# Kernel optimization log

Measured on AMD Instinct MI355X. Metric: run time of the kernel, lower is better.

The kernel has to match this reference:

```python
import jax, jax.numpy as jnp
import numpy as np

L, H, D, FF = 12, 12, 768, 3072          # ViT-B/16
PS, GRID = 16, 14
NP = GRID * GRID                          # 196 patches
NT = NP + 1                               # 197 tokens (cls + patches)
B = 64
NC = 100                                  # classes
POS_G = (0, 1)
POS_E = (2, 3, 4)
LEN_G, LEN_E = 5, 20
GL, EL = len(POS_G), len(POS_E)
E_POOL = 10                               # task_num


def _ln(x, g, b, eps=1e-6):
    m = x.mean(-1, keepdims=True)
    v = ((x - m) ** 2).mean(-1, keepdims=True)
    return (x - m) * jax.lax.rsqrt(v + eps) * g + b


def _mlp(x, w1, b1, w2, b2):
    return jax.nn.gelu(x @ w1.T + b1, approximate=False) @ w2.T + b2


def _attn(q, k, v):
    # q: [B,Nq,C], k/v: [B,Nk,C] (Nk may include prefix prompt tokens)
    Bq, Nq, C = q.shape
    hd = C // H
    q = q.reshape(Bq, Nq, H, hd).transpose(0, 2, 1, 3)
    k = k.reshape(Bq, -1, H, hd).transpose(0, 2, 1, 3)
    v = v.reshape(Bq, -1, H, hd).transpose(0, 2, 1, 3)
    a = jax.nn.softmax(jnp.einsum('bhqd,bhkd->bhqk', q, k) * (hd ** -0.5), axis=-1)
    o = jnp.einsum('bhqk,bhkd->bhqd', a, v)
    return o.transpose(0, 2, 1, 3).reshape(Bq, Nq, C)


def setup_inputs() -> dict:
    key = jax.random.key(0)
    ks = iter(jax.random.split(key, 24))
    s = 0.02
    return {
        'inputs':    jax.random.normal(next(ks), (B, 3, 224, 224), jnp.float32),
        'patch_w':   jax.random.normal(next(ks), (D, 3, PS, PS), jnp.float32) * s,
        'patch_b':   jnp.zeros((D,), jnp.float32),
        'cls_token': jax.random.normal(next(ks), (1, 1, D), jnp.float32) * s,
        'pos_embed': jax.random.normal(next(ks), (1, NT, D), jnp.float32) * s,
        'ln1_g':  jnp.ones((L, D), jnp.float32),
        'ln1_b':  jnp.zeros((L, D), jnp.float32),
        'qkv_w':  jax.random.normal(next(ks), (L, 3 * D, D), jnp.float32) * s,
        'qkv_b':  jnp.zeros((L, 3 * D), jnp.float32),
        'proj_w': jax.random.normal(next(ks), (L, D, D), jnp.float32) * s,
        'proj_b': jnp.zeros((L, D), jnp.float32),
        'ln2_g':  jnp.ones((L, D), jnp.float32),
        'ln2_b':  jnp.zeros((L, D), jnp.float32),
        'fc1_w':  jax.random.normal(next(ks), (L, FF, D), jnp.float32) * s,
        'fc1_b':  jnp.zeros((L, FF), jnp.float32),
        'fc2_w':  jax.random.normal(next(ks), (L, D, FF), jnp.float32) * s,
        'fc2_b':  jnp.zeros((L, D), jnp.float32),
        'norm_g': jnp.ones((D,), jnp.float32),
        'norm_b': jnp.zeros((D,), jnp.float32),
        'head_w': jax.random.normal(next(ks), (NC, D), jnp.float32) * s,
        'head_b': jnp.zeros((NC,), jnp.float32),
        'g_prompt': jax.random.normal(next(ks), (1, 2 * GL * LEN_G, D), jnp.float32) * s,
        'e_key':    jax.random.normal(next(ks), (E_POOL, D), jnp.float32),
        'e_prompt': jax.random.normal(next(ks), (E_POOL, 2 * EL * LEN_E, D), jnp.float32) * s,
    }


def _forward(inputs, patch_w, patch_b, cls_token, pos_embed, ln1_g, ln1_b,
             qkv_w, qkv_b, proj_w, proj_b, ln2_g, ln2_b, fc1_w, fc1_b,
             fc2_w, fc2_b, norm_g, norm_b, head_w, head_b,
             g_prompt, e_key, e_prompt):
    Bn = inputs.shape[0]
    # --- patch embed (conv k16 s16 == unfold + linear); under torch.no_grad ---
    x = inputs.reshape(Bn, 3, GRID, PS, GRID, PS).transpose(0, 2, 4, 1, 3, 5)
    x = x.reshape(Bn, NP, 3 * PS * PS) @ patch_w.reshape(D, -1).T + patch_b
    tok = jnp.concatenate([jnp.broadcast_to(cls_token, (Bn, 1, D)), x], axis=1)
    tok = jax.lax.stop_gradient(tok)  # token_appended computed in no_grad block
    # --- frozen query pass through plain ViT blocks ---
    q = tok + pos_embed
    for i in range(L):
        xn = _ln(q, ln1_g[i], ln1_b[i])
        qq, kk, vv = jnp.split(xn @ qkv_w[i].T + qkv_b[i], 3, axis=-1)
        q = q + _attn(qq, kk, vv) @ proj_w[i].T + proj_b[i]
        q = q + _mlp(_ln(q, ln2_g[i], ln2_b[i]), fc1_w[i], fc1_b[i], fc2_w[i], fc2_b[i])
    query = jax.lax.stop_gradient(_ln(q, norm_g, norm_b)[:, 0])  # [B, D]
    # --- prompt selection (eval path: cosine-sim top-1 from e-pool) ---
    qn = query / jnp.linalg.norm(query, axis=-1, keepdims=True)
    kn = e_key / jnp.linalg.norm(e_key, axis=-1, keepdims=True)
    idx = jnp.argmax(qn @ kn.T, axis=-1)                       # [B]
    cls_pe = pos_embed[0, 0]                                   # [D]
    g_p = jnp.broadcast_to(g_prompt[0].reshape(1, 2 * GL, LEN_G, D),
                           (Bn, 2 * GL, LEN_G, D)) + cls_pe
    e_p = e_prompt[idx].reshape(Bn, 2 * EL, LEN_E, D) + cls_pe
    # --- prefix-tuning pass: prompts concatenated to K/V only ---
    x = tok + pos_embed
    for n in range(L):
        xn = _ln(x, ln1_g[n], ln1_b[n])
        ks_, vs_ = [xn], [xn]
        if n in POS_G:
            j = POS_G.index(n)
            ks_.append(g_p[:, 2 * j]); vs_.append(g_p[:, 2 * j + 1])
        if n in POS_E:
            j = POS_E.index(n)
            ks_.append(e_p[:, 2 * j]); vs_.append(e_p[:, 2 * j + 1])
        xk = jnp.concatenate(ks_, axis=1) if len(ks_) > 1 else xn
        xv = jnp.concatenate(vs_, axis=1) if len(vs_) > 1 else xn
        qh = xn @ qkv_w[n][:D].T + qkv_b[n][:D]
        kh = xk @ qkv_w[n][D:2 * D].T + qkv_b[n][D:2 * D]
        vh = xv @ qkv_w[n][2 * D:].T + qkv_b[n][2 * D:]
        x = x + _attn(qh, kh, vh) @ proj_w[n].T + proj_b[n]
        x = x + _mlp(_ln(x, ln2_g[n], ln2_b[n]), fc1_w[n], fc1_b[n], fc2_w[n], fc2_b[n])
    x = _ln(x, norm_g, norm_b)
    return x[:, 0] @ head_w.T + head_b  # [B, NC]


def reference(inputs, patch_w, patch_b, cls_token, pos_embed, ln1_g, ln1_b,
              qkv_w, qkv_b, proj_w, proj_b, ln2_g, ln2_b, fc1_w, fc1_b,
              fc2_w, fc2_b, norm_g, norm_b, head_w, head_b,
              g_prompt, e_key, e_prompt):
    return _forward(inputs, patch_w, patch_b, cls_token, pos_embed, ln1_g, ln1_b,
                    qkv_w, qkv_b, proj_w, proj_b, ln2_g, ln2_b, fc1_w, fc1_b,
                    fc2_w, fc2_b, norm_g, norm_b, head_w, head_b,
                    g_prompt, e_key, e_prompt)
```

## Files before the change

kernel.cpp:

```cpp
#include <hip/hip_runtime.h>

typedef unsigned short ushort_t;
typedef __attribute__((ext_vector_type(8))) __bf16 bf16x8;
typedef __attribute__((ext_vector_type(4))) float f32x4;
typedef __attribute__((ext_vector_type(4))) unsigned int u32x4;
typedef __attribute__((ext_vector_type(4))) unsigned short u16x4;
typedef __attribute__((ext_vector_type(4))) float fl4;

#define AS1(p) ((const __attribute__((address_space(1))) void*)(p))
#define AS3(p) ((__attribute__((address_space(3))) void*)(p))

__device__ __forceinline__ ushort_t f2bf(float f) {
    unsigned u = __float_as_uint(f);
    u += 0x7FFFu + ((u >> 16) & 1u);
    return (ushort_t)(u >> 16);
}

__device__ __forceinline__ bf16x8 ld_bf8(const ushort_t* p) {
    return __builtin_bit_cast(bf16x8, *(const u32x4*)p);
}

__device__ __forceinline__ float gelu_f(float x) {
    float z = 1.5957691216057308f * (x + 0.044715f * x * x * x);
    float e = __expf(z);
    return x * e / (e + 1.f);
}

__global__ void cvt_kernel(const float* __restrict__ in, ushort_t* __restrict__ out, int n4)
{
    int i = blockIdx.x * 256 + threadIdx.x;
    if (i >= n4) return;
    fl4 f = ((const fl4*)in)[i];
    u16x4 h;
    h.x = f2bf(f.x); h.y = f2bf(f.y); h.z = f2bf(f.z); h.w = f2bf(f.w);
    ((u16x4*)out)[i] = h;
}

template<int OBF, int ADD, int GELU>
__global__ __launch_bounds__(256)
void gemm_kernel(const ushort_t* __restrict__ A, const ushort_t* __restrict__ W,
                 const float* __restrict__ bias, void* __restrict__ Cv,
                 int M, int N, int K, int ntiles)
{
    __shared__ ushort_t As[128 * 32];
    __shared__ ushort_t Ws[128 * 32];
    const int tid  = threadIdx.x;
    const int lane = tid & 63, wv = tid >> 6;
    const int quad = lane >> 4, l16 = lane & 15;

    const int mtiles = gridDim.x / ntiles;
    const int GM = 8;
    int gsz = GM * ntiles;
    int grp = blockIdx.x / gsz;
    int fm  = grp * GM;
    int gm  = min(GM, mtiles - fm);
    int ing = blockIdx.x - grp * gsz;
    const int m0 = (fm + ing % gm) * 128;
    const int n0 = (ing / gm) * 128;

    const int wm = (wv >> 1) * 64, wn = (wv & 1) * 64;

    f32x4 acc[4][4];
#pragma unroll
    for (int j = 0; j < 4; ++j)
#pragma unroll
        for (int i = 0; i < 4; ++i) acc[j][i] = (f32x4){0.f, 0.f, 0.f, 0.f};

    const int lr = lane >> 2, lc = (lane & 3) * 8;
    const ushort_t* gA0 = A + (size_t)(m0 + wv * 16 + lr) * K + lc;
    const ushort_t* gA1 = gA0 + (size_t)64 * K;
    const ushort_t* gW0 = W + (size_t)(n0 + wv * 16 + lr) * K + lc;
    const ushort_t* gW1 = gW0 + (size_t)64 * K;
    ushort_t* lA0 = As + wv * 512;
    ushort_t* lA1 = As + (wv + 4) * 512;
    ushort_t* lW0 = Ws + wv * 512;
    ushort_t* lW1 = Ws + (wv + 4) * 512;

    for (int kt = 0; kt < K; kt += 32) {
        __builtin_amdgcn_global_load_lds(AS1(gA0 + kt), AS3(lA0), 16, 0, 0);
        __builtin_amdgcn_global_load_lds(AS1(gA1 + kt), AS3(lA1), 16, 0, 0);
        __builtin_amdgcn_global_load_lds(AS1(gW0 + kt), AS3(lW0), 16, 0, 0);
        __builtin_amdgcn_global_load_lds(AS1(gW1 + kt), AS3(lW1), 16, 0, 0);
        __syncthreads();
        bf16x8 af[4], bfr[4];
#pragma unroll
        for (int i = 0; i < 4; ++i) af[i]  = ld_bf8(As + (wm + i * 16 + l16) * 32 + quad * 8);
#pragma unroll
        for (int j = 0; j < 4; ++j) bfr[j] = ld_bf8(Ws + (wn + j * 16 + l16) * 32 + quad * 8);
#pragma unroll
        for (int j = 0; j < 4; ++j)
#pragma unroll
            for (int i = 0; i < 4; ++i)
                acc[j][i] = __builtin_amdgcn_mfma_f32_16x16x32_bf16(bfr[j], af[i], acc[j][i], 0, 0, 0);
        __syncthreads();
    }

    float* Cf = (float*)Cv;
    ushort_t* Ch = (ushort_t*)Cv;
    fl4 bv[4];
#pragma unroll
    for (int j = 0; j < 4; ++j) bv[j] = *(const fl4*)(bias + n0 + wn + j * 16 + quad * 4);

#pragma unroll
    for (int i = 0; i < 4; ++i) {
        int m = m0 + wm + i * 16 + l16;
        if (m >= M) continue;
        size_t rowoff = (size_t)m * N;
#pragma unroll
        for (int j = 0; j < 4; ++j) {
            int nb = n0 + wn + j * 16 + quad * 4;
            float vals[4];
#pragma unroll
            for (int r = 0; r < 4; ++r) {
                float v = acc[j][i][r] + bv[j][r];
                if (GELU) v = gelu_f(v);
                vals[r] = v;
            }
            if (OBF) {
                u16x4 h;
                h.x = f2bf(vals[0]); h.y = f2bf(vals[1]);
                h.z = f2bf(vals[2]); h.w = f2bf(vals[3]);
                *(u16x4*)(Ch + rowoff + nb) = h;
            } else {
                fl4 o = {vals[0], vals[1], vals[2], vals[3]};
                if (ADD) {
                    fl4 c = *(const fl4*)(Cf + rowoff + nb);
                    o.x += c.x; o.y += c.y; o.z += c.z; o.w += c.w;
                }
                *(fl4*)(Cf + rowoff + nb) = o;
            }
        }
    }
}

__global__ __launch_bounds__(256)
void attn_kernel(const ushort_t* __restrict__ qkv, const ushort_t* __restrict__ pk,
                 const ushort_t* __restrict__ pv, int plen, int pbs,
                 ushort_t* __restrict__ out)
{
    __shared__ ushort_t KV[224 * 72];
    __shared__ ushort_t Ps[64 * 232];
    const int tid  = threadIdx.x;
    const int lane = tid & 63, wv = tid >> 6;
    const int quad = lane >> 4, l16 = lane & 15;
    const int b = blockIdx.x / 12, h = blockIdx.x % 12;
    const int q0 = blockIdx.y * 64;
    const int Nk = 197 + plen;

    for (int i = tid; i < 224 * 8; i += 256) {
        int tok = i >> 3, c = (i & 7) * 8;
        u32x4 v = (u32x4){0, 0, 0, 0};
        if (tok < 197)
            v = *(const u32x4*)(qkv + (size_t)(b * 197 + tok) * 2304 + 768 + h * 64 + c);
        else if (tok < Nk)
            v = *(const u32x4*)(pk + (size_t)(b * pbs + (tok - 197)) * 768 + h * 64 + c);
        *(u32x4*)(KV + tok * 72 + c) = v;
    }
    __syncthreads();

    bf16x8 qf0 = __builtin_bit_cast(bf16x8, (u32x4){0, 0, 0, 0});
    bf16x8 qf1 = qf0;
    int qrow = q0 + wv * 16 + l16;
    if (qrow < 197) {
        const ushort_t* qp = qkv + (size_t)(b * 197 + qrow) * 2304 + h * 64 + quad * 8;
        qf0 = ld_bf8(qp);
        qf1 = ld_bf8(qp + 32);
    }

    f32x4 sarr[14];
#pragma unroll
    for (int t = 0; t < 14; ++t) {
        f32x4 s = (f32x4){0.f, 0.f, 0.f, 0.f};
        bf16x8 k0 = ld_bf8(KV + (t * 16 + l16) * 72 + quad * 8);
        bf16x8 k1 = ld_bf8(KV + (t * 16 + l16) * 72 + 32 + quad * 8);
        s = __builtin_amdgcn_mfma_f32_16x16x32_bf16(qf0, k0, s, 0, 0, 0);
        s = __builtin_amdgcn_mfma_f32_16x16x32_bf16(qf1, k1, s, 0, 0, 0);
        if (t * 16 + l16 >= Nk) s = (f32x4){-1e30f, -1e30f, -1e30f, -1e30f};
        sarr[t] = s;
    }

    float mx[4] = {-1e30f, -1e30f, -1e30f, -1e30f};
#pragma unroll
    for (int t = 0; t < 14; ++t)
#pragma unroll
        for (int r = 0; r < 4; ++r) mx[r] = fmaxf(mx[r], sarr[t][r]);
#pragma unroll
    for (int off = 8; off >= 1; off >>= 1)
#pragma unroll
        for (int r = 0; r < 4; ++r) mx[r] = fmaxf(mx[r], __shfl_xor(mx[r], off));

    float sm[4] = {0.f, 0.f, 0.f, 0.f};
#pragma unroll
    for (int t = 0; t < 14; ++t)
#pragma unroll
        for (int r = 0; r < 4; ++r) {
            float p = __expf((sarr[t][r] - mx[r]) * 0.125f);
            sm[r] += p;
            Ps[(wv * 16 + quad * 4 + r) * 232 + t * 16 + l16] = f2bf(p);
        }
#pragma unroll
    for (int off = 8; off >= 1; off >>= 1)
#pragma unroll
        for (int r = 0; r < 4; ++r) sm[r] += __shfl_xor(sm[r], off);
    float rs[4];
#pragma unroll
    for (int r = 0; r < 4; ++r) rs[r] = 1.f / sm[r];
    __syncthreads();

    for (int i = tid; i < 224 * 8; i += 256) {
        int tok = i >> 3, c = (i & 7) * 8;
        u32x4 v = (u32x4){0, 0, 0, 0};
        if (tok < 197)
            v = *(const u32x4*)(qkv + (size_t)(b * 197 + tok) * 2304 + 1536 + h * 64 + c);
        else if (tok < Nk)
            v = *(const u32x4*)(pv + (size_t)(b * pbs + (tok - 197)) * 768 + h * 64 + c);
        ushort_t tmp[8];
        *(u32x4*)tmp = v;
#pragma unroll
        for (int jj = 0; jj < 8; ++jj) KV[(c + jj) * 232 + tok] = tmp[jj];
    }
    __syncthreads();

    f32x4 oc[4];
#pragma unroll
    for (int j = 0; j < 4; ++j) oc[j] = (f32x4){0.f, 0.f, 0.f, 0.f};
#pragma unroll
    for (int ks = 0; ks < 7; ++ks) {
        bf16x8 pf = ld_bf8(Ps + (wv * 16 + l16) * 232 + ks * 32 + quad * 8);
#pragma unroll
        for (int j = 0; j < 4; ++j) {
            bf16x8 vf = ld_bf8(KV + (j * 16 + l16) * 232 + ks * 32 + quad * 8);
            oc[j] = __builtin_amdgcn_mfma_f32_16x16x32_bf16(pf, vf, oc[j], 0, 0, 0);
        }
    }
#pragma unroll
    for (int j = 0; j < 4; ++j) {
        int hd = h * 64 + j * 16 + l16;
#pragma unroll
        for (int r = 0; r < 4; ++r) {
            int qr = q0 + wv * 16 + quad * 4 + r;
            if (qr < 197) out[(size_t)(b * 197 + qr) * 768 + hd] = f2bf(oc[j][r] * rs[r]);
        }
    }
}

__global__ __launch_bounds__(256)
void ln_kernel(const float* __restrict__ x, const float* __restrict__ g,
               const float* __restrict__ bt, ushort_t* __restrict__ out)
{
    const int row = blockIdx.x, tid = threadIdx.x;
    const float* xr = x + (size_t)row * 768;
    float v0 = xr[tid], v1 = xr[tid + 256], v2 = xr[tid + 512];
    float s = v0 + v1 + v2;
    float s2 = v0 * v0 + v1 * v1 + v2 * v2;
#pragma unroll
    for (int off = 32; off >= 1; off >>= 1) {
        s  += __shfl_xor(s, off);
        s2 += __shfl_xor(s2, off);
    }
    __shared__ float red[8];
    if ((tid & 63) == 0) { red[tid >> 6] = s; red[(tid >> 6) + 4] = s2; }
    __syncthreads();
    float S  = red[0] + red[1] + red[2] + red[3];
    float S2 = red[4] + red[5] + red[6] + red[7];
    float mean = S * (1.f / 768.f);
    float var  = fmaxf(S2 * (1.f / 768.f) - mean * mean, 0.f);
    float rstd = rsqrtf(var + 1e-6f);
    size_t o = (size_t)row * 768;
    out[o + tid]       = f2bf((v0 - mean) * rstd * g[tid]       + bt[tid]);
    out[o + tid + 256] = f2bf((v1 - mean) * rstd * g[tid + 256] + bt[tid + 256]);
    out[o + tid + 512] = f2bf((v2 - mean) * rstd * g[tid + 512] + bt[tid + 512]);
}

__global__ __launch_bounds__(256)
void ln_cls_kernel(const float* __restrict__ x, const float* __restrict__ g,
                   const float* __restrict__ bt, float* __restrict__ out)
{
    const int b = blockIdx.x, tid = threadIdx.x;
    const float* xr = x + (size_t)b * 197 * 768;
    float v0 = xr[tid], v1 = xr[tid + 256], v2 = xr[tid + 512];
    float s = v0 + v1 + v2;
    float s2 = v0 * v0 + v1 * v1 + v2 * v2;
#pragma unroll
    for (int off = 32; off >= 1; off >>= 1) {
        s  += __shfl_xor(s, off);
        s2 += __shfl_xor(s2, off);
    }
    __shared__ float red[8];
    if ((tid & 63) == 0) { red[tid >> 6] = s; red[(tid >> 6) + 4] = s2; }
    __syncthreads();
    float S  = red[0] + red[1] + red[2] + red[3];
    float S2 = red[4] + red[5] + red[6] + red[7];
    float mean = S * (1.f / 768.f);
    float var  = fmaxf(S2 * (1.f / 768.f) - mean * mean, 0.f);
    float rstd = rsqrtf(var + 1e-6f);
    out[b * 768 + tid]       = (v0 - mean) * rstd * g[tid]       + bt[tid];
    out[b * 768 + tid + 256] = (v1 - mean) * rstd * g[tid + 256] + bt[tid + 256];
    out[b * 768 + tid + 512] = (v2 - mean) * rstd * g[tid + 512] + bt[tid + 512];
}

__device__ __forceinline__ float block_sum(float v, float* red, int tid)
{
#pragma unroll
    for (int off = 32; off >= 1; off >>= 1) v += __shfl_xor(v, off);
    __syncthreads();
    if ((tid & 63) == 0) red[tid >> 6] = v;
    __syncthreads();
    return red[0] + red[1] + red[2] + red[3];
}

__global__ __launch_bounds__(256)
void select_kernel(const float* __restrict__ q, const float* __restrict__ ek,
                   int* __restrict__ idx)
{
    __shared__ float red[4];
    int b = blockIdx.x, tid = threadIdx.x;
    const float* qr = q + b * 768;
    float q0 = qr[tid], q1 = qr[tid + 256], q2 = qr[tid + 512];
    float qq = block_sum(q0 * q0 + q1 * q1 + q2 * q2, red, tid);
    float best = -1e30f; int bi = 0;
    for (int p = 0; p < 10; ++p) {
        const float* kr = ek + p * 768;
        float k0 = kr[tid], k1 = kr[tid + 256], k2 = kr[tid + 512];
        float dt = block_sum(q0 * k0 + q1 * k1 + q2 * k2, red, tid);
        float kk = block_sum(k0 * k0 + k1 * k1 + k2 * k2, red, tid);
        float sim = dt / sqrtf(qq * kk);
        if (sim > best) { best = sim; bi = p; }
    }
    if (tid == 0) idx[b] = bi;
}

__global__ void im2col_kernel(const float* __restrict__ in, ushort_t* __restrict__ out)
{
    int i = blockIdx.x * 256 + threadIdx.x;
    int k = i % 768, m = i / 768;
    int b = m / 196, p = m % 196;
    int gy = p / 14, gx = p % 14;
    int c = k >> 8, r = k & 255, py = r >> 4, px = r & 15;
    out[i] = f2bf(in[(size_t)((b * 3 + c) * 224 + gy * 16 + py) * 224 + gx * 16 + px]);
}

__global__ void assemble_kernel(const float* __restrict__ pt, const float* __restrict__ cls,
                                const float* __restrict__ pos, float* __restrict__ x0)
{
    int i = blockIdx.x * 256 + threadIdx.x;
    int d = i % 768, m = i / 768;
    int bb = m / 197, t = m % 197;
    float v = (t == 0) ? cls[d] : pt[(size_t)(bb * 196 + t - 1) * 768 + d];
    x0[i] = v + pos[t * 768 + d];
}

__global__ void build_gtok_kernel(const float* __restrict__ gp, const float* __restrict__ pos,
                                  ushort_t* __restrict__ out, int sel)
{
    int i = blockIdx.x * 256 + threadIdx.x;
    int d = i % 768, t = i / 768;
    out[i] = f2bf(gp[(sel * 5 + t) * 768 + d] + pos[d]);
}

__global__ void build_etok_kernel(const float* __restrict__ ep, const float* __restrict__ pos,
                                  const int* __restrict__ idx, ushort_t* __restrict__ out, int sel)
{
    int i = blockIdx.x * 256 + threadIdx.x;
    int d = i % 768;
    int t = (i / 768) % 20;
    int b = i / (768 * 20);
    out[i] = f2bf(ep[((size_t)idx[b] * 120 + sel * 20 + t) * 768 + d] + pos[d]);
}

__global__ __launch_bounds__(256)
void head_kernel(const float* __restrict__ cl, const float* __restrict__ hw,
                 const float* __restrict__ hb, float* __restrict__ out)
{
    __shared__ float row[768];
    int b = blockIdx.x, tid = threadIdx.x;
    row[tid]       = cl[b * 768 + tid];
    row[tid + 256] = cl[b * 768 + tid + 256];
    row[tid + 512] = cl[b * 768 + tid + 512];
    __syncthreads();
    for (int c = tid; c < 100; c += 256) {
        float a = hb[c];
        for (int d = 0; d < 768; ++d) a += row[d] * hw[(size_t)c * 768 + d];
        out[b * 100 + c] = a;
    }
}

extern "C" void kernel_launch(void* const* d_in, const int* in_sizes, int n_in,
                              void* d_out, int out_size, void* d_ws, size_t ws_size,
                              hipStream_t stream)
{
    const float* inputs   = (const float*)d_in[0];
    const float* patch_w  = (const float*)d_in[1];
    const float* patch_b  = (const float*)d_in[2];
    const float* cls_tok  = (const float*)d_in[3];
    const float* pos_emb  = (const float*)d_in[4];
    const float* ln1_g    = (const float*)d_in[5];
    const float* ln1_b    = (const float*)d_in[6];
    const float* qkv_w    = (const float*)d_in[7];
    const float* qkv_b    = (const float*)d_in[8];
    const float* proj_w   = (const float*)d_in[9];
    const float* proj_b   = (const float*)d_in[10];
    const float* ln2_g    = (const float*)d_in[11];
    const float* ln2_b    = (const float*)d_in[12];
    const float* fc1_w    = (const float*)d_in[13];
    const float* fc1_b    = (const float*)d_in[14];
    const float* fc2_w    = (const float*)d_in[15];
    const float* fc2_b    = (const float*)d_in[16];
    const float* norm_g   = (const float*)d_in[17];
    const float* norm_b   = (const float*)d_in[18];
    const float* head_w   = (const float*)d_in[19];
    const float* head_b   = (const float*)d_in[20];
    const float* g_prompt = (const float*)d_in[21];
    const float* e_key    = (const float*)d_in[22];
    const float* e_prompt = (const float*)d_in[23];

    char* wp = (char*)d_ws;
    auto carve = [&](size_t bytes) {
        char* p = wp;
        wp += (bytes + 255) & ~(size_t)255;
        return p;
    };
    ushort_t* wqkv = (ushort_t*)carve(12ull * 2304 * 768 * 2);
    ushort_t* wprj = (ushort_t*)carve(12ull * 768 * 768 * 2);
    ushort_t* wfc1 = (ushort_t*)carve(12ull * 3072 * 768 * 2);
    ushort_t* wfc2 = (ushort_t*)carve(12ull * 768 * 3072 * 2);
    ushort_t* wpat = (ushort_t*)carve(768ull * 768 * 2);
    float*    x     = (float*)   carve(12608ull * 768 * 4);
    ushort_t* xn    = (ushort_t*)carve(12672ull * 768 * 2);
    ushort_t* big   = (ushort_t*)carve(12672ull * 3072 * 2);
    ushort_t* ptk   = (ushort_t*)carve(1280ull * 768 * 2);
    ushort_t* pK    = (ushort_t*)carve(1280ull * 768 * 2);
    ushort_t* pV    = (ushort_t*)carve(1280ull * 768 * 2);
    float*    query = (float*)   carve(64ull * 768 * 4);
    float*    clsln = (float*)   carve(64ull * 768 * 4);
    int*      idx   = (int*)     carve(256);
    (void)ws_size; (void)in_sizes; (void)n_in; (void)out_size;

    cvt_kernel<<<20736, 256, 0, stream>>>(qkv_w,   wqkv, 5308416);
    cvt_kernel<<< 6912, 256, 0, stream>>>(proj_w,  wprj, 1769472);
    cvt_kernel<<<27648, 256, 0, stream>>>(fc1_w,   wfc1, 7077888);
    cvt_kernel<<<27648, 256, 0, stream>>>(fc2_w,   wfc2, 7077888);
    cvt_kernel<<<  576, 256, 0, stream>>>(patch_w, wpat, 147456);

    for (int pass = 0; pass < 2; ++pass) {
        im2col_kernel<<<37632, 256, 0, stream>>>(inputs, xn);
        gemm_kernel<0, 0, 0><<<98 * 6, 256, 0, stream>>>(xn, wpat, patch_b,
                                                         (void*)big, 12544, 768, 768, 6);
        assemble_kernel<<<37824, 256, 0, stream>>>((const float*)big, cls_tok, pos_emb, x);

        for (int l = 0; l < 12; ++l) {
            ln_kernel<<<12608, 256, 0, stream>>>(x, ln1_g + l * 768, ln1_b + l * 768, xn);
            gemm_kernel<1, 0, 0><<<99 * 18, 256, 0, stream>>>(
                xn, wqkv + (size_t)l * 2304 * 768, qkv_b + l * 2304, big, 12608, 2304, 768, 18);

            const ushort_t* pkp = nullptr; const ushort_t* pvp = nullptr;
            int plen = 0, pbs = 0;
            if (pass == 1 && l < 5) {
                const ushort_t* Wk = wqkv + (size_t)l * 2304 * 768 + 768ull * 768;
                const ushort_t* Wv = wqkv + (size_t)l * 2304 * 768 + 1536ull * 768;
                const float* bk = qkv_b + l * 2304 + 768;
                const float* bv = qkv_b + l * 2304 + 1536;
                if (l < 2) {
                    build_gtok_kernel<<<15, 256, 0, stream>>>(g_prompt, pos_emb, ptk, 2 * l);
                    gemm_kernel<1, 0, 0><<<6, 256, 0, stream>>>(ptk, Wk, bk, pK, 5, 768, 768, 6);
                    build_gtok_kernel<<<15, 256, 0, stream>>>(g_prompt, pos_emb, ptk, 2 * l + 1);
                    gemm_kernel<1, 0, 0><<<6, 256, 0, stream>>>(ptk, Wv, bv, pV, 5, 768, 768, 6);
                    pkp = pK; pvp = pV; plen = 5; pbs = 0;
                } else {
                    int j = l - 2;
                    build_etok_kernel<<<3840, 256, 0, stream>>>(e_prompt, pos_emb, idx, ptk, 2 * j);
                    gemm_kernel<1, 0, 0><<<10 * 6, 256, 0, stream>>>(ptk, Wk, bk, pK, 1280, 768, 768, 6);
                    build_etok_kernel<<<3840, 256, 0, stream>>>(e_prompt, pos_emb, idx, ptk, 2 * j + 1);
                    gemm_kernel<1, 0, 0><<<10 * 6, 256, 0, stream>>>(ptk, Wv, bv, pV, 1280, 768, 768, 6);
                    pkp = pK; pvp = pV; plen = 20; pbs = 20;
                }
            }
            attn_kernel<<<dim3(768, 4), 256, 0, stream>>>(big, pkp, pvp, plen, pbs, xn);
            gemm_kernel<0, 1, 0><<<99 * 6, 256, 0, stream>>>(
                xn, wprj + (size_t)l * 768 * 768, proj_b + l * 768, x, 12608, 768, 768, 6);
            ln_kernel<<<12608, 256, 0, stream>>>(x, ln2_g + l * 768, ln2_b + l * 768, xn);
            gemm_kernel<1, 0, 1><<<99 * 24, 256, 0, stream>>>(
                xn, wfc1 + (size_t)l * 3072 * 768, fc1_b + l * 3072, big, 12608, 3072, 768, 24);
            gemm_kernel<0, 1, 0><<<99 * 6, 256, 0, stream>>>(
                big, wfc2 + (size_t)l * 768 * 3072, fc2_b + l * 768, x, 12608, 768, 3072, 6);
        }
        if (pass == 0) {
            ln_cls_kernel<<<64, 256, 0, stream>>>(x, norm_g, norm_b, query);
            select_kernel<<<64, 256, 0, stream>>>(query, e_key, idx);
        } else {
            ln_cls_kernel<<<64, 256, 0, stream>>>(x, norm_g, norm_b, clsln);
            head_kernel<<<64, 256, 0, stream>>>(clsln, head_w, head_b, (float*)d_out);
        }
    }
}
```

Before: 12.26 ms.

## Triple-buffer GEMM LDS loads and compute patch embedding once for both passes

The GEMM main loop now uses three LDS stages, prefetching two k-tiles ahead and synchronising with a single vmcnt wait plus barrier per iteration instead of two __syncthreads. This lets global-to-LDS loads overlap MFMA work. Separately, the patch-embedding im2col, GEMM and assemble steps run once into a saved buffer, which is copied into x at the start of each pass instead of being recomputed. The pipeline triples LDS use, which may lower occupancy, and the stage-prefetch tail issues redundant loads from k=0.

```diff
diff --git a/kernel.cpp b/kernel.cpp
--- a/kernel.cpp
+++ b/kernel.cpp
@@ -42,8 +42,8 @@
                  const float* __restrict__ bias, void* __restrict__ Cv,
                  int M, int N, int K, int ntiles)
 {
-    __shared__ ushort_t As[128 * 32];
-    __shared__ ushort_t Ws[128 * 32];
+    __shared__ ushort_t As[3 * 4096];
+    __shared__ ushort_t Ws[3 * 4096];
     const int tid  = threadIdx.x;
     const int lane = tid & 63, wv = tid >> 6;
     const int quad = lane >> 4, l16 = lane & 15;
@@ -71,29 +71,37 @@
     const ushort_t* gA1 = gA0 + (size_t)64 * K;
     const ushort_t* gW0 = W + (size_t)(n0 + wv * 16 + lr) * K + lc;
     const ushort_t* gW1 = gW0 + (size_t)64 * K;
-    ushort_t* lA0 = As + wv * 512;
-    ushort_t* lA1 = As + (wv + 4) * 512;
-    ushort_t* lW0 = Ws + wv * 512;
-    ushort_t* lW1 = Ws + (wv + 4) * 512;
-
-    for (int kt = 0; kt < K; kt += 32) {
-        __builtin_amdgcn_global_load_lds(AS1(gA0 + kt), AS3(lA0), 16, 0, 0);
-        __builtin_amdgcn_global_load_lds(AS1(gA1 + kt), AS3(lA1), 16, 0, 0);
-        __builtin_amdgcn_global_load_lds(AS1(gW0 + kt), AS3(lW0), 16, 0, 0);
-        __builtin_amdgcn_global_load_lds(AS1(gW1 + kt), AS3(lW1), 16, 0, 0);
-        __syncthreads();
+
+    const int niter = K >> 5;
+
+    auto issue = [&](int t) {
+        int kt = t << 5;
+        if (kt >= K) kt = 0;
+        int bo = (t % 3) * 4096;
+        __builtin_amdgcn_global_load_lds(AS1(gA0 + kt), AS3(As + bo + wv * 512), 16, 0, 0);
+        __builtin_amdgcn_global_load_lds(AS1(gA1 + kt), AS3(As + bo + (wv + 4) * 512), 16, 0, 0);
+        __builtin_amdgcn_global_load_lds(AS1(gW0 + kt), AS3(Ws + bo + wv * 512), 16, 0, 0);
+        __builtin_amdgcn_global_load_lds(AS1(gW1 + kt), AS3(Ws + bo + (wv + 4) * 512), 16, 0, 0);
+    };
+
+    issue(0);
+    issue(1);
+    for (int it = 0; it < niter; ++it) {
+        asm volatile("s_waitcnt vmcnt(4)\n\ts_barrier" ::: "memory");
+        issue(it + 2);
+        const int bo = (it % 3) * 4096;
         bf16x8 af[4], bfr[4];
 #pragma unroll
-        for (int i = 0; i < 4; ++i) af[i]  = ld_bf8(As + (wm + i * 16 + l16) * 32 + quad * 8);
-#pragma unroll
-        for (int j = 0; j < 4; ++j) bfr[j] = ld_bf8(Ws + (wn + j * 16 + l16) * 32 + quad * 8);
+        for (int i = 0; i < 4; ++i) af[i]  = ld_bf8(As + bo + (wm + i * 16 + l16) * 32 + quad * 8);
+#pragma unroll
+        for (int j = 0; j < 4; ++j) bfr[j] = ld_bf8(Ws + bo + (wn + j * 16 + l16) * 32 + quad * 8);
 #pragma unroll
         for (int j = 0; j < 4; ++j)
 #pragma unroll
             for (int i = 0; i < 4; ++i)
                 acc[j][i] = __builtin_amdgcn_mfma_f32_16x16x32_bf16(bfr[j], af[i], acc[j][i], 0, 0, 0);
-        __syncthreads();
-    }
+    }
+    asm volatile("s_waitcnt vmcnt(0)" ::: "memory");
 
     float* Cf = (float*)Cv;
     ushort_t* Ch = (ushort_t*)Cv;
@@ -426,6 +434,7 @@
     ushort_t* wfc2 = (ushort_t*)carve(12ull * 768 * 3072 * 2);
     ushort_t* wpat = (ushort_t*)carve(768ull * 768 * 2);
     float*    x     = (float*)   carve(12608ull * 768 * 4);
+    float*    x0    = (float*)   carve(12608ull * 768 * 4);
     ushort_t* xn    = (ushort_t*)carve(12672ull * 768 * 2);
     ushort_t* big   = (ushort_t*)carve(12672ull * 3072 * 2);
     ushort_t* ptk   = (ushort_t*)carve(1280ull * 768 * 2);
@@ -442,11 +451,13 @@
     cvt_kernel<<<27648, 256, 0, stream>>>(fc2_w,   wfc2, 7077888);
     cvt_kernel<<<  576, 256, 0, stream>>>(patch_w, wpat, 147456);
 
+    im2col_kernel<<<37632, 256, 0, stream>>>(inputs, xn);
+    gemm_kernel<0, 0, 0><<<98 * 6, 256, 0, stream>>>(xn, wpat, patch_b,
+                                                     (void*)big, 12544, 768, 768, 6);
+    assemble_kernel<<<37824, 256, 0, stream>>>((const float*)big, cls_tok, pos_emb, x0);
+
     for (int pass = 0; pass < 2; ++pass) {
-        im2col_kernel<<<37632, 256, 0, stream>>>(inputs, xn);
-        gemm_kernel<0, 0, 0><<<98 * 6, 256, 0, stream>>>(xn, wpat, patch_b,
-                                                         (void*)big, 12544, 768, 768, 6);
-        assemble_kernel<<<37824, 256, 0, stream>>>((const float*)big, cls_tok, pos_emb, x);
+        hipMemcpyAsync(x, x0, 12608ull * 768 * 4, hipMemcpyDeviceToDevice, stream);
 
         for (int l = 0; l < 12; ++l) {
             ln_kernel<<<12608, 256, 0, stream>>>(x, ln1_g + l * 768, ln1_b + l * 768, xn);
```

Measured after the change: 14.34 ms. 16.9% more time.
